# Optimization experiments

Hardware: AMD Instinct MI355X
Metric: run time of the kernel (lower is better)

## Reference

```python
import jax, jax.numpy as jnp
import numpy as np

PARTIAL_DATA_THRESHOLD = 0.1  # threshold on squared NN distance (ChamferDistance returns squared dists)


def setup_inputs() -> dict:
    key = jax.random.key(0)
    k1, k2 = jax.random.split(key)
    scan_vertices = jax.random.normal(k1, (50000, 3), dtype=jnp.float32)      # N x 3
    template_vertices = jax.random.normal(k2, (6890, 3), dtype=jnp.float32)   # M x 3
    return {"scan_vertices": scan_vertices, "template_vertices": template_vertices}


def reference(scan_vertices, template_vertices):
    # Directional (template -> scan) Chamfer: for each template point, squared
    # distance to nearest scan point; then sum distances below threshold.
    # d2[m, n] = |t_m|^2 + |s_n|^2 - 2 t_m . s_n
    t_sq = jnp.sum(template_vertices * template_vertices, axis=-1)            # [M]
    s_sq = jnp.sum(scan_vertices * scan_vertices, axis=-1)                    # [N]
    cross = jnp.einsum('md,nd->mn', template_vertices, scan_vertices)         # [M, N]
    d2 = t_sq[:, None] + s_sq[None, :] - 2.0 * cross                          # [M, N]
    template2scan = jnp.min(d2, axis=1)                                       # [M]
    mask = template2scan < PARTIAL_DATA_THRESHOLD
    return jnp.sum(jnp.where(mask, template2scan, 0.0))
```

## Files before the change

### kernel.cpp

```cpp
#include <hip/hip_runtime.h>
#include <hip/hip_bf16.h>

#define BLK 256
#define SPLITS 24
#define FRTOT 1584
#define FPS (FRTOT / SPLITS)
#define NSLOT (FRTOT * 32)
#define THRESH 0.1f
#define KEY_MAX 0xFFFFFFFFu
#define ONE_BF ((unsigned short)0x3F80)

typedef __attribute__((ext_vector_type(8))) short short8;
typedef __attribute__((ext_vector_type(16))) float floatx16;

__device__ __forceinline__ unsigned short f2bf(float x) {
    unsigned u = __float_as_uint(x);
    unsigned r = u + 0x7FFFu + ((u >> 16) & 1u);
    return (unsigned short)(r >> 16);
}
__device__ __forceinline__ float bf2f(unsigned short h) {
    return __uint_as_float(((unsigned)h) << 16);
}

__device__ __forceinline__ unsigned f2key(float f) {
    unsigned b = __float_as_uint(f);
    return (b & 0x80000000u) ? ~b : (b | 0x80000000u);
}
__device__ __forceinline__ float key2f(unsigned k) {
    return __uint_as_float((k & 0x80000000u) ? (k & 0x7FFFFFFFu) : ~k);
}

template <int CTRL>
__device__ __forceinline__ float dpp_ror_min(float v) {
    const int i = __float_as_int(v);
    const int p = __builtin_amdgcn_update_dpp(i, i, CTRL, 0xF, 0xF, false);
    return fminf(v, __int_as_float(p));
}

__global__ __launch_bounds__(BLK) void pdl_prep(const float* __restrict__ scan,
                                                uint4* __restrict__ fragbuf,
                                                unsigned* __restrict__ gmin,
                                                float* __restrict__ out,
                                                int N, int Mpad) {
    const int n = blockIdx.x * BLK + threadIdx.x;
    if (n == 0) out[0] = 0.0f;
    if (n < Mpad) gmin[n] = KEY_MAX;
    if (n >= NSLOT) return;

    unsigned short k[16];
    if (n < N) {
        const float x = scan[3 * n + 0], y = scan[3 * n + 1], z = scan[3 * n + 2];
        const float s2 = fmaf(x, x, fmaf(y, y, z * z));
        const float cx = -2.0f * x, cy = -2.0f * y, cz = -2.0f * z;
        const unsigned short xh = f2bf(cx); const unsigned short xl = f2bf(cx - bf2f(xh));
        const unsigned short yh = f2bf(cy); const unsigned short yl = f2bf(cy - bf2f(yh));
        const unsigned short zh = f2bf(cz); const unsigned short zl = f2bf(cz - bf2f(zh));
        const unsigned short wh = f2bf(s2); const unsigned short wl = f2bf(s2 - bf2f(wh));
        k[0] = xh; k[1] = xl; k[2] = xh; k[3] = xl;
        k[4] = yh; k[5] = yl; k[6] = yh; k[7] = yl;
        k[8] = zh; k[9] = zl; k[10] = zh; k[11] = zl;
        k[12] = ONE_BF; k[13] = ONE_BF;
        k[14] = wh; k[15] = wl;
    } else {
#pragma unroll
        for (int i = 0; i < 16; ++i) k[i] = 0;
        k[12] = ONE_BF; k[13] = ONE_BF;
        k[14] = f2bf(1e30f); k[15] = 0;
    }

    const int g = n >> 5, c = n & 31;
    uint4 lo, hi;
    lo.x = (unsigned)k[0] | ((unsigned)k[1] << 16);
    lo.y = (unsigned)k[2] | ((unsigned)k[3] << 16);
    lo.z = (unsigned)k[4] | ((unsigned)k[5] << 16);
    lo.w = (unsigned)k[6] | ((unsigned)k[7] << 16);
    hi.x = (unsigned)k[8] | ((unsigned)k[9] << 16);
    hi.y = (unsigned)k[10] | ((unsigned)k[11] << 16);
    hi.z = (unsigned)k[12] | ((unsigned)k[13] << 16);
    hi.w = (unsigned)k[14] | ((unsigned)k[15] << 16);
    fragbuf[(size_t)g * 64 + c] = lo;
    fragbuf[(size_t)g * 64 + 32 + c] = hi;
}

__global__ __launch_bounds__(BLK, 4) void pdl_main(const float* __restrict__ tmpl,
                                                   const uint4* __restrict__ fragbuf,
                                                   unsigned* __restrict__ gmin,
                                                   int M) {
    const int tid = threadIdx.x;
    const int wave = tid >> 6, lane = tid & 63;

    const int mbase = (blockIdx.y * 4 + wave) * 32;
    short8 A;
    {
        int m = mbase + (lane & 31);
        if (m > M - 1) m = M - 1;
        const float x = tmpl[3 * m + 0], y = tmpl[3 * m + 1], z = tmpl[3 * m + 2];
        const float t2 = fmaf(x, x, fmaf(y, y, z * z));
        const unsigned short xh = f2bf(x); const unsigned short xl = f2bf(x - bf2f(xh));
        const unsigned short yh = f2bf(y); const unsigned short yl = f2bf(y - bf2f(yh));
        const unsigned short zh = f2bf(z); const unsigned short zl = f2bf(z - bf2f(zh));
        const unsigned short wh = f2bf(t2); const unsigned short wl = f2bf(t2 - bf2f(wh));
        const bool hi = (lane >= 32);
        A[0] = (short)(hi ? zh : xh);
        A[1] = (short)(hi ? zh : xh);
        A[2] = (short)(hi ? zl : xl);
        A[3] = (short)(hi ? zl : xl);
        A[4] = (short)(hi ? wh : yh);
        A[5] = (short)(hi ? wl : yh);
        A[6] = (short)(hi ? ONE_BF : yl);
        A[7] = (short)(hi ? ONE_BF : yl);
    }

    floatx16 mn, zacc;
#pragma unroll
    for (int r = 0; r < 16; ++r) { mn[r] = 3e30f; zacc[r] = 0.0f; }

    const uint4* fb = fragbuf + (size_t)(blockIdx.x * FPS) * 64 + lane;

    union U { uint4 u; short8 s; };
    uint4 p0 = fb[0];
    uint4 p1 = fb[64];
#pragma unroll 1
    for (int f = 0; f < FPS; f += 2) {
        U c0, c1; c0.u = p0; c1.u = p1;
        p0 = fb[(size_t)(f + 2) * 64];
        p1 = fb[(size_t)(f + 3) * 64];
        const floatx16 d0 = __builtin_amdgcn_mfma_f32_32x32x16_bf16(A, c0.s, zacc, 0, 0, 0);
        const floatx16 d1 = __builtin_amdgcn_mfma_f32_32x32x16_bf16(A, c1.s, zacc, 0, 0, 0);
#pragma unroll
        for (int r = 0; r < 16; ++r)
            mn[r] = fminf(fminf(d0[r], d1[r]), mn[r]);
    }

#pragma unroll
    for (int r = 0; r < 16; ++r) {
        float v = mn[r];
        v = dpp_ror_min<0x128>(v);
        v = dpp_ror_min<0x124>(v);
        v = dpp_ror_min<0x122>(v);
        v = dpp_ror_min<0x121>(v);
        const int sw = __builtin_amdgcn_ds_swizzle(__float_as_int(v), 0x401F);
        v = fminf(v, __int_as_float(sw));
        if ((lane & 31) == 0) {
            const int row = (r & 3) + 8 * (r >> 2) + ((lane >> 5) << 2);
            atomicMin(&gmin[mbase + row], f2key(v));
        }
    }
}

__global__ __launch_bounds__(BLK) void pdl_final(const unsigned* __restrict__ gmin,
                                                 float* __restrict__ out, int M) {
    const int m = blockIdx.x * BLK + threadIdx.x;
    float s = 0.0f;
    if (m < M) {
        const float v = key2f(gmin[m]);
        if (v < THRESH) s = v;
    }
#pragma unroll
    for (int off = 32; off > 0; off >>= 1) s += __shfl_down(s, off, 64);

    __shared__ float ls[BLK / 64];
    const int lane = threadIdx.x & 63;
    const int w = threadIdx.x >> 6;
    if (lane == 0) ls[w] = s;
    __syncthreads();
    if (threadIdx.x == 0) {
        float t = 0.0f;
#pragma unroll
        for (int i = 0; i < BLK / 64; ++i) t += ls[i];
        atomicAdd(out, t);
    }
}

extern "C" void kernel_launch(void* const* d_in, const int* in_sizes, int n_in,
                              void* d_out, int out_size, void* d_ws, size_t ws_size,
                              hipStream_t stream) {
    const float* scan = (const float*)d_in[0];
    const float* tmpl = (const float*)d_in[1];
    float* out = (float*)d_out;

    const int N = in_sizes[0] / 3;
    const int M = in_sizes[1] / 3;

    const int tGroups = (M + 127) / 128;
    const int Mpad = ((M + 31) / 32) * 32 + 128;

    unsigned* gmin = (unsigned*)d_ws;
    uint4* fragbuf = (uint4*)((char*)d_ws + 65536);

    pdl_prep<<<(NSLOT + BLK - 1) / BLK, BLK, 0, stream>>>(scan, fragbuf, gmin,
                                                          out, N, Mpad);

    dim3 grid(SPLITS, tGroups);
    pdl_main<<<grid, BLK, 0, stream>>>(tmpl, fragbuf, gmin, M);

    pdl_final<<<(M + BLK - 1) / BLK, BLK, 0, stream>>>(gmin, out, M);
}
```

Before: 78.98 us.

## Swap MFMA operand roles and register-block template tiles per wave

After: 73.03 us. 7.5% less time.

```diff
diff --git a/kernel.cpp b/kernel.cpp
--- a/kernel.cpp
+++ b/kernel.cpp
@@ -2,10 +2,15 @@
 #include <hip/hip_bf16.h>
 
 #define BLK 256
-#define SPLITS 24
+#define WPB 4
+#define TB 12
+#define TSPLITS 18
+#define SA 11
+#define SSPLITS 144
 #define FRTOT 1584
-#define FPS (FRTOT / SPLITS)
 #define NSLOT (FRTOT * 32)
+#define MFR 216
+#define MPAD (MFR * 32)
 #define THRESH 0.1f
 #define KEY_MAX 0xFFFFFFFFu
 #define ONE_BF ((unsigned short)0x3F80)
@@ -30,21 +35,50 @@
     return __uint_as_float((k & 0x80000000u) ? (k & 0x7FFFFFFFu) : ~k);
 }
 
-template <int CTRL>
-__device__ __forceinline__ float dpp_ror_min(float v) {
-    const int i = __float_as_int(v);
-    const int p = __builtin_amdgcn_update_dpp(i, i, CTRL, 0xF, 0xF, false);
-    return fminf(v, __int_as_float(p));
-}
-
 __global__ __launch_bounds__(BLK) void pdl_prep(const float* __restrict__ scan,
-                                                uint4* __restrict__ fragbuf,
+                                                const float* __restrict__ tmpl,
+                                                uint4* __restrict__ afrag,
+                                                uint4* __restrict__ bfrag,
                                                 unsigned* __restrict__ gmin,
                                                 float* __restrict__ out,
-                                                int N, int Mpad) {
+                                                int N, int M) {
     const int n = blockIdx.x * BLK + threadIdx.x;
     if (n == 0) out[0] = 0.0f;
-    if (n < Mpad) gmin[n] = KEY_MAX;
+
+    if (n < MPAD) {
+        gmin[n] = KEY_MAX;
+        unsigned short q[16];
+        if (n < M) {
+            const float x = tmpl[3 * n + 0], y = tmpl[3 * n + 1], z = tmpl[3 * n + 2];
+            const float t2 = fmaf(x, x, fmaf(y, y, z * z));
+            const unsigned short xh = f2bf(x); const unsigned short xl = f2bf(x - bf2f(xh));
+            const unsigned short yh = f2bf(y); const unsigned short yl = f2bf(y - bf2f(yh));
+            const unsigned short zh = f2bf(z); const unsigned short zl = f2bf(z - bf2f(zh));
+            const unsigned short wh = f2bf(t2); const unsigned short wl = f2bf(t2 - bf2f(wh));
+            q[0] = xh; q[1] = xh; q[2] = xl; q[3] = xl;
+            q[4] = yh; q[5] = yh; q[6] = yl; q[7] = yl;
+            q[8] = zh; q[9] = zh; q[10] = zl; q[11] = zl;
+            q[12] = wh; q[13] = wl;
+            q[14] = ONE_BF; q[15] = ONE_BF;
+        } else {
+#pragma unroll
+            for (int i = 0; i < 16; ++i) q[i] = 0;
+            q[14] = ONE_BF; q[15] = ONE_BF;
+        }
+        const int g = n >> 5, c = n & 31;
+        uint4 lo, hi;
+        lo.x = (unsigned)q[0] | ((unsigned)q[1] << 16);
+        lo.y = (unsigned)q[2] | ((unsigned)q[3] << 16);
+        lo.z = (unsigned)q[4] | ((unsigned)q[5] << 16);
+        lo.w = (unsigned)q[6] | ((unsigned)q[7] << 16);
+        hi.x = (unsigned)q[8] | ((unsigned)q[9] << 16);
+        hi.y = (unsigned)q[10] | ((unsigned)q[11] << 16);
+        hi.z = (unsigned)q[12] | ((unsigned)q[13] << 16);
+        hi.w = (unsigned)q[14] | ((unsigned)q[15] << 16);
+        bfrag[(size_t)g * 64 + c] = lo;
+        bfrag[(size_t)g * 64 + 32 + c] = hi;
+    }
+
     if (n >= NSLOT) return;
 
     unsigned short k[16];
@@ -78,74 +112,71 @@
     hi.y = (unsigned)k[10] | ((unsigned)k[11] << 16);
     hi.z = (unsigned)k[12] | ((unsigned)k[13] << 16);
     hi.w = (unsigned)k[14] | ((unsigned)k[15] << 16);
-    fragbuf[(size_t)g * 64 + c] = lo;
-    fragbuf[(size_t)g * 64 + 32 + c] = hi;
-}
-
-__global__ __launch_bounds__(BLK, 4) void pdl_main(const float* __restrict__ tmpl,
-                                                   const uint4* __restrict__ fragbuf,
-                                                   unsigned* __restrict__ gmin,
-                                                   int M) {
+    afrag[(size_t)g * 64 + c] = lo;
+    afrag[(size_t)g * 64 + 32 + c] = hi;
+}
+
+__global__ __launch_bounds__(BLK, 3) void pdl_main(const uint4* __restrict__ afrag,
+                                                   const uint4* __restrict__ bfrag,
+                                                   unsigned* __restrict__ gmin) {
     const int tid = threadIdx.x;
     const int wave = tid >> 6, lane = tid & 63;
-
-    const int mbase = (blockIdx.y * 4 + wave) * 32;
-    short8 A;
-    {
-        int m = mbase + (lane & 31);
-        if (m > M - 1) m = M - 1;
-        const float x = tmpl[3 * m + 0], y = tmpl[3 * m + 1], z = tmpl[3 * m + 2];
-        const float t2 = fmaf(x, x, fmaf(y, y, z * z));
-        const unsigned short xh = f2bf(x); const unsigned short xl = f2bf(x - bf2f(xh));
-        const unsigned short yh = f2bf(y); const unsigned short yl = f2bf(y - bf2f(yh));
-        const unsigned short zh = f2bf(z); const unsigned short zl = f2bf(z - bf2f(zh));
-        const unsigned short wh = f2bf(t2); const unsigned short wl = f2bf(t2 - bf2f(wh));
-        const bool hi = (lane >= 32);
-        A[0] = (short)(hi ? zh : xh);
-        A[1] = (short)(hi ? zh : xh);
-        A[2] = (short)(hi ? zl : xl);
-        A[3] = (short)(hi ? zl : xl);
-        A[4] = (short)(hi ? wh : yh);
-        A[5] = (short)(hi ? wl : yh);
-        A[6] = (short)(hi ? ONE_BF : yl);
-        A[7] = (short)(hi ? ONE_BF : yl);
-    }
-
-    floatx16 mn, zacc;
-#pragma unroll
-    for (int r = 0; r < 16; ++r) { mn[r] = 3e30f; zacc[r] = 0.0f; }
-
-    const uint4* fb = fragbuf + (size_t)(blockIdx.x * FPS) * 64 + lane;
+    const int tsplit = blockIdx.x;
+    const int ssplit = blockIdx.y * WPB + wave;
+
+    __shared__ unsigned lmin[TB * 32];
+#pragma unroll 2
+    for (int i = tid; i < TB * 32; i += BLK) lmin[i] = KEY_MAX;
 
     union U { uint4 u; short8 s; };
-    uint4 p0 = fb[0];
-    uint4 p1 = fb[64];
+
+    const uint4* bb = bfrag + (size_t)(tsplit * TB) * 64 + lane;
+    U B[TB];
+#pragma unroll
+    for (int j = 0; j < TB; ++j) B[j].u = bb[(size_t)j * 64];
+
+    float mn[TB];
+#pragma unroll
+    for (int j = 0; j < TB; ++j) mn[j] = 3e30f;
+
+    floatx16 zacc;
+#pragma unroll
+    for (int r = 0; r < 16; ++r) zacc[r] = 0.0f;
+
+    __syncthreads();
+
+    const uint4* ab = afrag + (size_t)(ssplit * SA) * 64 + lane;
+    uint4 p = ab[0];
 #pragma unroll 1
-    for (int f = 0; f < FPS; f += 2) {
-        U c0, c1; c0.u = p0; c1.u = p1;
-        p0 = fb[(size_t)(f + 2) * 64];
-        p1 = fb[(size_t)(f + 3) * 64];
-        const floatx16 d0 = __builtin_amdgcn_mfma_f32_32x32x16_bf16(A, c0.s, zacc, 0, 0, 0);
-        const floatx16 d1 = __builtin_amdgcn_mfma_f32_32x32x16_bf16(A, c1.s, zacc, 0, 0, 0);
-#pragma unroll
-        for (int r = 0; r < 16; ++r)
-            mn[r] = fminf(fminf(d0[r], d1[r]), mn[r]);
-    }
-
-#pragma unroll
-    for (int r = 0; r < 16; ++r) {
-        float v = mn[r];
-        v = dpp_ror_min<0x128>(v);
-        v = dpp_ror_min<0x124>(v);
-        v = dpp_ror_min<0x122>(v);
-        v = dpp_ror_min<0x121>(v);
-        const int sw = __builtin_amdgcn_ds_swizzle(__float_as_int(v), 0x401F);
-        v = fminf(v, __int_as_float(sw));
-        if ((lane & 31) == 0) {
-            const int row = (r & 3) + 8 * (r >> 2) + ((lane >> 5) << 2);
-            atomicMin(&gmin[mbase + row], f2key(v));
+    for (int f = 0; f < SA; ++f) {
+        U a; a.u = p;
+        p = ab[(size_t)(f + 1) * 64];
+#pragma unroll
+        for (int j = 0; j < TB; ++j) {
+            const floatx16 d =
+                __builtin_amdgcn_mfma_f32_32x32x16_bf16(a.s, B[j].s, zacc, 0, 0, 0);
+            const float t0 = fminf(fminf(d[0], d[1]), d[2]);
+            const float t1 = fminf(fminf(d[3], d[4]), d[5]);
+            const float t2 = fminf(fminf(d[6], d[7]), d[8]);
+            const float t3 = fminf(fminf(d[9], d[10]), d[11]);
+            const float t4 = fminf(fminf(d[12], d[13]), d[14]);
+            const float u0 = fminf(fminf(t0, t1), t2);
+            const float u1 = fminf(fminf(t3, t4), d[15]);
+            mn[j] = fminf(fminf(u0, u1), mn[j]);
         }
     }
+
+#pragma unroll
+    for (int j = 0; j < TB; ++j) {
+        const float o = __shfl_xor(mn[j], 32, 64);
+        const float v = fminf(mn[j], o);
+        if (lane < 32) atomicMin(&lmin[j * 32 + lane], f2key(v));
+    }
+    __syncthreads();
+
+    const int mbase = tsplit * (TB * 32);
+#pragma unroll 2
+    for (int i = tid; i < TB * 32; i += BLK) atomicMin(&gmin[mbase + i], lmin[i]);
 }
 
 __global__ __launch_bounds__(BLK) void pdl_final(const unsigned* __restrict__ gmin,
@@ -182,17 +213,15 @@
     const int N = in_sizes[0] / 3;
     const int M = in_sizes[1] / 3;
 
-    const int tGroups = (M + 127) / 128;
-    const int Mpad = ((M + 31) / 32) * 32 + 128;
-
     unsigned* gmin = (unsigned*)d_ws;
-    uint4* fragbuf = (uint4*)((char*)d_ws + 65536);
-
-    pdl_prep<<<(NSLOT + BLK - 1) / BLK, BLK, 0, stream>>>(scan, fragbuf, gmin,
-                                                          out, N, Mpad);
-
-    dim3 grid(SPLITS, tGroups);
-    pdl_main<<<grid, BLK, 0, stream>>>(tmpl, fragbuf, gmin, M);
+    uint4* afrag = (uint4*)((char*)d_ws + 65536);
+    uint4* bfrag = (uint4*)((char*)d_ws + 65536 + (size_t)(FRTOT + 2) * 1024);
+
+    pdl_prep<<<(NSLOT + BLK - 1) / BLK, BLK, 0, stream>>>(scan, tmpl, afrag, bfrag,
+                                                          gmin, out, N, M);
+
+    dim3 grid(TSPLITS, SSPLITS / WPB);
+    pdl_main<<<grid, BLK, 0, stream>>>(afrag, bfrag, gmin);
 
     pdl_final<<<(M + BLK - 1) / BLK, BLK, 0, stream>>>(gmin, out, M);
 }
```
